# Optimization experiments

Hardware: AMD Instinct MI355X
Metric: run time of the kernel (lower is better)

The kernel has to match this reference:

```python
import jax, jax.numpy as jnp
import numpy as np

N_NODES = 100000


def gcn_layer(x, W, b, src, dst):
    """PyG GCNConv: xw = x @ W; symmetric norm with self-loops; out = agg + b."""
    n = x.shape[0]
    xw = x @ W  # [N, F_out]
    # degree over destination nodes, including self-loop (+1)
    deg = jax.ops.segment_sum(jnp.ones_like(dst, dtype=xw.dtype), dst, num_segments=n) + 1.0
    dinv = jax.lax.rsqrt(deg)  # [N]
    coef = dinv[src] * dinv[dst]  # [E]
    msgs = xw[src] * coef[:, None]  # [E, F_out] gather + scale
    agg = jax.ops.segment_sum(msgs, dst, num_segments=n)
    agg = agg + xw * (dinv * dinv)[:, None]  # self-loop contribution
    return agg + b


def setup_inputs() -> dict:
    key = jax.random.key(0)
    ks = jax.random.split(key, 8)
    N, E, C_in, H = N_NODES, 800000, 256, 128
    x = jax.random.normal(ks[0], (N, C_in), dtype=jnp.float32)
    edge_index = jax.random.randint(ks[1], (2, E), 0, N, dtype=jnp.int64)
    def glorot(k, fan_in, fan_out):
        s = jnp.sqrt(2.0 / (fan_in + fan_out))
        return jax.random.normal(k, (fan_in, fan_out), dtype=jnp.float32) * s
    return {
        "x": x,
        "edge_index": edge_index,
        "W1": glorot(ks[2], C_in, H),
        "b1": jnp.zeros((H,), jnp.float32),
        "W2": glorot(ks[3], H, H // 2),
        "b2": jnp.zeros((H // 2,), jnp.float32),
        "W3": glorot(ks[4], H // 2, H // 4),
        "b3": jnp.zeros((H // 4,), jnp.float32),
    }


def reference(x, edge_index, W1, b1, W2, b2, W3, b3):
    src, dst = edge_index[0], edge_index[1]
    x = jax.nn.relu(gcn_layer(x, W1, b1, src, dst))
    x = jax.nn.relu(gcn_layer(x, W2, b2, src, dst))
    x = jax.nn.relu(gcn_layer(x, W3, b3, src, dst))
    return x
```

## Files before the change

kernel.cpp:

```cpp
#include <hip/hip_runtime.h>
#include <hip/hip_bf16.h>
#include <math.h>

typedef __attribute__((ext_vector_type(8))) short s16x8;
typedef __attribute__((ext_vector_type(4))) float f32x4;

constexpr int CAP = 40;

__device__ __forceinline__ unsigned short f2bf(float f) {
    unsigned int u = __float_as_uint(f);
    u += 0x7fffu + ((u >> 16) & 1u);
    return (unsigned short)(u >> 16);
}

__device__ __forceinline__ unsigned int pk2bf(float a, float b) {
    __hip_bfloat162 h = __float22bfloat162_rn(make_float2(a, b));
    return *(unsigned int*)&h;
}

__device__ __forceinline__ float dinv_of(int c) {
    return rsqrtf((float)min(c, CAP) + 1.0f);
}


__global__ void prep_kernel(int* __restrict__ cursor, int N,
                            const float* __restrict__ W1, const float* __restrict__ W2,
                            const float* __restrict__ W3, unsigned short* __restrict__ Wt1,
                            unsigned short* __restrict__ Wt2, unsigned short* __restrict__ Wt3) {
    int i = blockIdx.x * blockDim.x + threadIdx.x;
    if (i < N) cursor[i] = 0;
    if (i < 32768) {
        int k = i >> 7, n = i & 127;
        Wt1[(size_t)n * 264 + k] = f2bf(W1[i]);
    } else if (i < 40960) {
        int j = i - 32768, k = j >> 6, n = j & 63;
        Wt2[(size_t)n * 136 + k] = f2bf(W2[j]);
    } else if (i < 43008) {
        int j = i - 40960, k = j >> 5, n = j & 31;
        Wt3[(size_t)n * 72 + k] = f2bf(W3[j]);
    }
}


__device__ __forceinline__ s16x8 cvt8(const float4& u, const float4& v) {
    union { unsigned int w[4]; s16x8 s; } cb;
    cb.w[0] = pk2bf(u.x, u.y);
    cb.w[1] = pk2bf(u.z, u.w);
    cb.w[2] = pk2bf(v.x, v.y);
    cb.w[3] = pk2bf(v.z, v.w);
    return cb.s;
}

__global__ __launch_bounds__(256) void gemm1_fill_kernel(const float* __restrict__ A,
                                                         const unsigned short* __restrict__ Bt,
                                                         unsigned short* __restrict__ C, int M,
                                                         const int* __restrict__ src,
                                                         const int* __restrict__ dst,
                                                         int* __restrict__ cursor,
                                                         int* __restrict__ pack, int E, int GB) {
    constexpr int KP = 72;
    constexpr int AP = 68;
    __shared__ unsigned short Wlds[128 * KP];
    __shared__ float Alds[64 * AP];

    int tid = threadIdx.x;
    int wv = tid >> 6, lane = tid & 63;
    int r0 = blockIdx.x * 64;
    int lr = lane & 15, kg = lane >> 4;

    f32x4 acc[8] = {};

#pragma unroll
    for (int ch = 0; ch < 4; ++ch) {
        if (ch) __syncthreads();
#pragma unroll
        for (int it = 0; it < 4; ++it) {
            int u = it * 256 + tid;
            int n = u >> 3, c8 = u & 7;
            *(uint4*)&Wlds[n * KP + c8 * 8] =
                *(const uint4*)&Bt[(size_t)n * 264 + ch * 64 + c8 * 8];
        }
#pragma unroll
        for (int pss = 0; pss < 4; ++pss) {
            int row = pss * 16 + (tid >> 4);
            int c4 = (tid & 15) * 4;
            int gr = min(r0 + row, M - 1);
            *(float4*)&Alds[row * AP + c4] = *(const float4*)&A[(size_t)gr * 256 + ch * 64 + c4];
        }
        __syncthreads();
#pragma unroll
        for (int ks = 0; ks < 2; ++ks) {
            const float* ap = &Alds[(wv * 16 + lr) * AP + ks * 32 + kg * 8];
            s16x8 a0 = cvt8(*(const float4*)ap, *(const float4*)(ap + 4));
#pragma unroll
            for (int ni = 0; ni < 8; ++ni) {
                const s16x8 b = *(const s16x8*)&Wlds[(ni * 16 + lr) * KP + ks * 32 + kg * 8];
                acc[ni] = __builtin_amdgcn_mfma_f32_16x16x32_bf16(a0, b, acc[ni], 0, 0, 0);
            }
        }
    }

#pragma unroll
    for (int r = 0; r < 4; ++r) {
        int row = r0 + wv * 16 + kg * 4 + r;
        if (row < M) {
#pragma unroll
            for (int ni = 0; ni < 8; ++ni)
                C[(size_t)row * 128 + ni * 16 + lr] = f2bf(acc[ni][r]);
        }
    }

    for (int e = blockIdx.x * 256 + tid; e < E; e += GB * 256) {
        int s = src[e], d = dst[e];
        int pos = atomicAdd(&cursor[d], 1);
        if (pos < CAP) pack[(size_t)d * CAP + pos] = s;
    }
}


template <int F, int VPL>
__device__ __forceinline__ void gather_node(const unsigned short* __restrict__ xw,
                                            const int* __restrict__ cursor,
                                            const int* __restrict__ pack,
                                            const float* __restrict__ bias,
                                            int wid, int f0, float* o) {
    auto loadrow = [&](const unsigned short* r, float* y) {
        if constexpr (VPL == 8) {
            uint4 b = *(const uint4*)(r + f0);
            y[0] = __uint_as_float(b.x << 16);
            y[1] = __uint_as_float(b.x & 0xffff0000u);
            y[2] = __uint_as_float(b.y << 16);
            y[3] = __uint_as_float(b.y & 0xffff0000u);
            y[4] = __uint_as_float(b.z << 16);
            y[5] = __uint_as_float(b.z & 0xffff0000u);
            y[6] = __uint_as_float(b.w << 16);
            y[7] = __uint_as_float(b.w & 0xffff0000u);
        } else if constexpr (VPL == 4) {
            uint2 b = *(const uint2*)(r + f0);
            y[0] = __uint_as_float(b.x << 16);
            y[1] = __uint_as_float(b.x & 0xffff0000u);
            y[2] = __uint_as_float(b.y << 16);
            y[3] = __uint_as_float(b.y & 0xffff0000u);
        } else {
            unsigned int b = *(const unsigned int*)(r + f0);
            y[0] = __uint_as_float(b << 16);
            y[1] = __uint_as_float(b & 0xffff0000u);
        }
    };

    int cw = cursor[wid];
    float dnd = dinv_of(cw);
    int cnt = min(cw, CAP);
    float acc[VPL], y[8][VPL];
    loadrow(xw + (size_t)wid * F, y[0]);
#pragma unroll
    for (int q = 0; q < VPL; ++q) acc[q] = dnd * y[0][q];

    int beg = wid * CAP;
    int j = 0;
    for (; j + 7 < cnt; j += 8) {
        int pp[8];
#pragma unroll
        for (int u = 0; u < 8; ++u) pp[u] = pack[beg + j + u];
        float cc[8];
#pragma unroll
        for (int u = 0; u < 8; ++u) cc[u] = dinv_of(cursor[pp[u]]);
#pragma unroll
        for (int u = 0; u < 8; ++u) loadrow(xw + (size_t)pp[u] * F, y[u]);
#pragma unroll
        for (int u = 0; u < 8; ++u) {
#pragma unroll
            for (int q = 0; q < VPL; ++q) acc[q] += y[u][q] * cc[u];
        }
    }
    for (; j + 3 < cnt; j += 4) {
        int pp[4];
#pragma unroll
        for (int u = 0; u < 4; ++u) pp[u] = pack[beg + j + u];
        float cc[4];
#pragma unroll
        for (int u = 0; u < 4; ++u) cc[u] = dinv_of(cursor[pp[u]]);
#pragma unroll
        for (int u = 0; u < 4; ++u) loadrow(xw + (size_t)pp[u] * F, y[u]);
#pragma unroll
        for (int u = 0; u < 4; ++u) {
#pragma unroll
            for (int q = 0; q < VPL; ++q) acc[q] += y[u][q] * cc[u];
        }
    }
    for (; j < cnt; ++j) {
        int s = pack[beg + j];
        float c0 = dinv_of(cursor[s]);
        loadrow(xw + (size_t)s * F, y[0]);
#pragma unroll
        for (int q = 0; q < VPL; ++q) acc[q] += y[0][q] * c0;
    }

#pragma unroll
    for (int q = 0; q < VPL; ++q) o[q] = fmaxf(fmaf(dnd, acc[q], bias[f0 + q]), 0.0f);
}


template <int K, int N>
__global__ __launch_bounds__(256) void mfma_gemm_kernel(const unsigned short* __restrict__ A,
                                                        const unsigned short* __restrict__ Bt,
                                                        unsigned short* __restrict__ C, int M) {
    constexpr int KP = K + 8;
    constexpr int KSTEPS = K / 32;
    constexpr int NFRAG = N / 16;
    __shared__ unsigned short Blds[N * KP];

    int tid = threadIdx.x;
    for (int off = tid * 16; off < N * KP * 2; off += 256 * 16)
        *(float4*)((char*)Blds + off) = *(const float4*)((const char*)Bt + off);
    __syncthreads();

    int wv = tid >> 6, lane = tid & 63;
    int r0 = blockIdx.x * 64 + wv * 16;
    int lr = lane & 15, kg = lane >> 4;
    int ra = min(r0 + lr, M - 1);

    f32x4 acc[NFRAG] = {};
    const unsigned short* ah = A + (size_t)ra * K + kg * 8;

#pragma unroll
    for (int ks = 0; ks < KSTEPS; ++ks) {
        s16x8 a0 = *(const s16x8*)(ah + ks * 32);
#pragma unroll
        for (int ni = 0; ni < NFRAG; ++ni) {
            const s16x8 b = *(const s16x8*)&Blds[(ni * 16 + lr) * KP + kg * 8 + ks * 32];
            acc[ni] = __builtin_amdgcn_mfma_f32_16x16x32_bf16(a0, b, acc[ni], 0, 0, 0);
        }
    }

#pragma unroll
    for (int r = 0; r < 4; ++r) {
        int row = r0 + kg * 4 + r;
        if (row < M) {
#pragma unroll
            for (int ni = 0; ni < NFRAG; ++ni)
                C[(size_t)row * N + ni * 16 + lr] = f2bf(acc[ni][r]);
        }
    }
}


template <int F, int GPW, int VPL, bool OUT_BF16>
__global__ __launch_bounds__(256) void gather_kernel(const unsigned short* __restrict__ xw,
                                                     const int* __restrict__ cursor,
                                                     const int* __restrict__ pack,
                                                     const float* __restrict__ bias,
                                                     void* __restrict__ outv, int N) {
    constexpr int LPG = 64 / GPW;
    static_assert(LPG * VPL == F, "lane layout must cover F");
    int wave = blockIdx.x * 4 + (threadIdx.x >> 6);
    int lane = threadIdx.x & 63;
    int wid = wave * GPW + lane / LPG;
    int gl = lane % LPG;
    if (wid >= N) return;
    const int f0 = gl * VPL;

    float o[VPL];
    gather_node<F, VPL>(xw, cursor, pack, bias, wid, f0, o);

    if constexpr (OUT_BF16) {
        unsigned short* op = (unsigned short*)outv + (size_t)wid * F + f0;
        if constexpr (VPL == 8) {
            *(uint4*)op = make_uint4(pk2bf(o[0], o[1]), pk2bf(o[2], o[3]),
                                     pk2bf(o[4], o[5]), pk2bf(o[6], o[7]));
        } else if constexpr (VPL == 4) {
            *(uint2*)op = make_uint2(pk2bf(o[0], o[1]), pk2bf(o[2], o[3]));
        } else {
            *(unsigned int*)op = pk2bf(o[0], o[1]);
        }
    } else {
        float* op = (float*)outv + (size_t)wid * F + f0;
        if constexpr (VPL == 4) {
            *(float4*)op = make_float4(o[0], o[1], o[2], o[3]);
        } else {
            *(float2*)op = make_float2(o[0], o[1]);
        }
    }
}


extern "C" void kernel_launch(void* const* d_in, const int* in_sizes, int n_in,
                              void* d_out, int out_size, void* d_ws, size_t ws_size,
                              hipStream_t stream) {
    const float* x = (const float*)d_in[0];
    const int* edge = (const int*)d_in[1];
    const float* W1 = (const float*)d_in[2];
    const float* b1 = (const float*)d_in[3];
    const float* W2 = (const float*)d_in[4];
    const float* b2 = (const float*)d_in[5];
    const float* W3 = (const float*)d_in[6];
    const float* b3 = (const float*)d_in[7];

    const int C_IN = 256, H1 = 128;
    const int N = in_sizes[0] / C_IN;
    const int E = in_sizes[1] / 2;
    const int* srcp = edge;
    const int* dstp = edge + E;

    char* p = (char*)d_ws;
    size_t o = 0;
    auto alloc = [&](size_t bytes) -> void* {
        void* r = p + o;
        o = (o + bytes + 255) & ~(size_t)255;
        return r;
    };
    int*   cursor = (int*)alloc((size_t)N * 4);
    int*   pack   = (int*)alloc((size_t)N * CAP * 4);
    unsigned short* Wt1 = (unsigned short*)alloc((size_t)128 * 264 * 2);
    unsigned short* Wt2 = (unsigned short*)alloc((size_t)64 * 136 * 2);
    unsigned short* Wt3 = (unsigned short*)alloc((size_t)32 * 72 * 2);
    unsigned short* xwb = (unsigned short*)alloc((size_t)N * H1 * 2);
    unsigned short* act = (unsigned short*)alloc((size_t)N * H1 * 2);
    float* out = (float*)d_out;

    const int GEMM_BLOCKS = (N + 63) / 64;

    prep_kernel<<<(N + 255) / 256, 256, 0, stream>>>(cursor, N, W1, W2, W3, Wt1, Wt2, Wt3);

    gemm1_fill_kernel<<<GEMM_BLOCKS, 256, 0, stream>>>(x, Wt1, xwb, N, srcp, dstp, cursor,
                                                       pack, E, GEMM_BLOCKS);

    gather_kernel<128, 4, 8, true><<<(N + 15) / 16, 256, 0, stream>>>(xwb, cursor, pack, b1, act, N);
    mfma_gemm_kernel<128, 64><<<GEMM_BLOCKS, 256, 0, stream>>>(act, Wt2, xwb, N);
    gather_kernel<64, 4, 4, true><<<(N + 15) / 16, 256, 0, stream>>>(xwb, cursor, pack, b2, act, N);
    mfma_gemm_kernel<64, 32><<<GEMM_BLOCKS, 256, 0, stream>>>(act, Wt3, xwb, N);
    gather_kernel<32, 4, 2, false><<<(N + 15) / 16, 256, 0, stream>>>(xwb, cursor, pack, b3, out, N);
}
```

Baseline: 169.8 us.

## Fuse neighbor gather with next-layer MFMA GEMM through LDS

Replaces the separate gather and GEMM kernels for layers 2 and 3 with one kernel. Each 16-node block aggregates neighbor rows into an LDS tile and multiplies it by the staged weight matrix using MFMA. This removes the write and re-read of the intermediate activation buffer and two kernel launches. In exchange, each 16-row block reloads the whole weight matrix into LDS, and only NFRAGS of the four waves do MFMA work, so the weight-load traffic and idle waves may offset the savings.

```diff
diff --git a/kernel.cpp b/kernel.cpp
--- a/kernel.cpp
+++ b/kernel.cpp
@@ -201,45 +201,57 @@
 }
 
 
-template <int K, int N>
-__global__ __launch_bounds__(256) void mfma_gemm_kernel(const unsigned short* __restrict__ A,
-                                                        const unsigned short* __restrict__ Bt,
-                                                        unsigned short* __restrict__ C, int M) {
-    constexpr int KP = K + 8;
-    constexpr int KSTEPS = K / 32;
-    constexpr int NFRAG = N / 16;
-    __shared__ unsigned short Blds[N * KP];
+template <int F_IN, int F_OUT>
+__global__ __launch_bounds__(256) void gather_gemm_kernel(
+    const unsigned short* __restrict__ xw, const int* __restrict__ cursor,
+    const int* __restrict__ pack, const float* __restrict__ bias,
+    const unsigned short* __restrict__ Wt, unsigned short* __restrict__ C, int N) {
+    constexpr int VPL = F_IN / 16;
+    constexpr int KP = F_IN + 8;
+    constexpr int KSTEPS = F_IN / 32;
+    constexpr int NFRAGS = F_OUT / 16;
+    __shared__ unsigned short Wlds[F_OUT * KP];
+    __shared__ unsigned short Alds[16 * KP];
 
     int tid = threadIdx.x;
-    for (int off = tid * 16; off < N * KP * 2; off += 256 * 16)
-        *(float4*)((char*)Blds + off) = *(const float4*)((const char*)Bt + off);
+    int wv = tid >> 6, lane = tid & 63;
+    int blk16 = blockIdx.x * 16;
+    int lr = lane & 15, kg = lane >> 4;
+
+    for (int off = tid * 16; off < F_OUT * KP * 2; off += 256 * 16)
+        *(uint4*)((char*)Wlds + off) = *(const uint4*)((const char*)Wt + off);
+
+    {
+        int nl = wv * 4 + (lane >> 4);
+        int wid = blk16 + nl;
+        const int f0 = lr * VPL;
+        if (wid < N) {
+            float o[VPL];
+            gather_node<F_IN, VPL>(xw, cursor, pack, bias, wid, f0, o);
+            unsigned short* ap = &Alds[nl * KP + f0];
+            if constexpr (VPL == 8) {
+                *(uint4*)ap = make_uint4(pk2bf(o[0], o[1]), pk2bf(o[2], o[3]),
+                                         pk2bf(o[4], o[5]), pk2bf(o[6], o[7]));
+            } else {
+                *(uint2*)ap = make_uint2(pk2bf(o[0], o[1]), pk2bf(o[2], o[3]));
+            }
+        }
+    }
     __syncthreads();
 
-    int wv = tid >> 6, lane = tid & 63;
-    int r0 = blockIdx.x * 64 + wv * 16;
-    int lr = lane & 15, kg = lane >> 4;
-    int ra = min(r0 + lr, M - 1);
-
-    f32x4 acc[NFRAG] = {};
-    const unsigned short* ah = A + (size_t)ra * K + kg * 8;
-
-#pragma unroll
-    for (int ks = 0; ks < KSTEPS; ++ks) {
-        s16x8 a0 = *(const s16x8*)(ah + ks * 32);
-#pragma unroll
-        for (int ni = 0; ni < NFRAG; ++ni) {
-            const s16x8 b = *(const s16x8*)&Blds[(ni * 16 + lr) * KP + kg * 8 + ks * 32];
-            acc[ni] = __builtin_amdgcn_mfma_f32_16x16x32_bf16(a0, b, acc[ni], 0, 0, 0);
-        }
-    }
-
-#pragma unroll
-    for (int r = 0; r < 4; ++r) {
-        int row = r0 + kg * 4 + r;
-        if (row < M) {
-#pragma unroll
-            for (int ni = 0; ni < NFRAG; ++ni)
-                C[(size_t)row * N + ni * 16 + lr] = f2bf(acc[ni][r]);
+    if (wv < NFRAGS) {
+        f32x4 acc = {};
+#pragma unroll
+        for (int ks = 0; ks < KSTEPS; ++ks) {
+            const s16x8 a = *(const s16x8*)&Alds[lr * KP + ks * 32 + kg * 8];
+            const s16x8 b = *(const s16x8*)&Wlds[(wv * 16 + lr) * KP + ks * 32 + kg * 8];
+            acc = __builtin_amdgcn_mfma_f32_16x16x32_bf16(a, b, acc, 0, 0, 0);
+        }
+#pragma unroll
+        for (int r = 0; r < 4; ++r) {
+            int row = blk16 + kg * 4 + r;
+            if (row < N)
+                C[(size_t)row * F_OUT + wv * 16 + lr] = f2bf(acc[r]);
         }
     }
 }
@@ -296,7 +308,7 @@
     const float* W3 = (const float*)d_in[6];
     const float* b3 = (const float*)d_in[7];
 
-    const int C_IN = 256, H1 = 128;
+    const int C_IN = 256;
     const int N = in_sizes[0] / C_IN;
     const int E = in_sizes[1] / 2;
     const int* srcp = edge;
@@ -314,20 +326,23 @@
     unsigned short* Wt1 = (unsigned short*)alloc((size_t)128 * 264 * 2);
     unsigned short* Wt2 = (unsigned short*)alloc((size_t)64 * 136 * 2);
     unsigned short* Wt3 = (unsigned short*)alloc((size_t)32 * 72 * 2);
-    unsigned short* xwb = (unsigned short*)alloc((size_t)N * H1 * 2);
-    unsigned short* act = (unsigned short*)alloc((size_t)N * H1 * 2);
+    unsigned short* xwb = (unsigned short*)alloc((size_t)N * 128 * 2);
+    unsigned short* xw2 = (unsigned short*)alloc((size_t)N * 64 * 2);
+    unsigned short* xw3 = (unsigned short*)alloc((size_t)N * 32 * 2);
     float* out = (float*)d_out;
 
     const int GEMM_BLOCKS = (N + 63) / 64;
+    const int FUSE_BLOCKS = (N + 15) / 16;
 
     prep_kernel<<<(N + 255) / 256, 256, 0, stream>>>(cursor, N, W1, W2, W3, Wt1, Wt2, Wt3);
 
     gemm1_fill_kernel<<<GEMM_BLOCKS, 256, 0, stream>>>(x, Wt1, xwb, N, srcp, dstp, cursor,
                                                        pack, E, GEMM_BLOCKS);
 
-    gather_kernel<128, 4, 8, true><<<(N + 15) / 16, 256, 0, stream>>>(xwb, cursor, pack, b1, act, N);
-    mfma_gemm_kernel<128, 64><<<GEMM_BLOCKS, 256, 0, stream>>>(act, Wt2, xwb, N);
-    gather_kernel<64, 4, 4, true><<<(N + 15) / 16, 256, 0, stream>>>(xwb, cursor, pack, b2, act, N);
-    mfma_gemm_kernel<64, 32><<<GEMM_BLOCKS, 256, 0, stream>>>(act, Wt3, xwb, N);
-    gather_kernel<32, 4, 2, false><<<(N + 15) / 16, 256, 0, stream>>>(xwb, cursor, pack, b3, out, N);
-}
+    gather_gemm_kernel<128, 64><<<FUSE_BLOCKS, 256, 0, stream>>>(xwb, cursor, pack, b1, Wt2,
+                                                                 xw2, N);
+    gather_gemm_kernel<64, 32><<<FUSE_BLOCKS, 256, 0, stream>>>(xw2, cursor, pack, b2, Wt3,
+                                                                xw3, N);
+    gather_kernel<32, 4, 2, false><<<(N + 15) / 16, 256, 0, stream>>>(xw3, cursor, pack, b3,
+                                                                      out, N);
+}
```

New measurement: 163.7 us. 3.6% less time.
